# Kernel tuning notes

Measured on AMD Instinct MI355X. Metric: run time of the kernel, lower is better.

The kernel has to match this reference:

```python
import jax, jax.numpy as jnp
import numpy as np

B, T, D = 4, 4096, 512
H, L = 8, 6
HD = D // H
BS = 64          # block_size
MLP = 2048
VOCAB = 96000
MAX_SCALE = 10000.0
LN_EPS = 1e-6


def _sinusoidal_pe(length, dim, max_scale=MAX_SCALE):
    # flax common_layers sinusoidal init (concat sin|cos halves)
    pos = np.arange(length)[:, None].astype(np.float32)
    div = np.exp(np.arange(0, dim, 2).astype(np.float32) * -(np.log(max_scale) / dim))
    pe = np.zeros((length, dim), dtype=np.float32)
    pe[:, : dim // 2] = np.sin(pos * div)
    pe[:, dim // 2:] = np.cos(pos * div)
    return jnp.asarray(pe)

_PE = _sinusoidal_pe(T, D)


def layer_norm(x, scale, bias):
    m = jnp.mean(x, axis=-1, keepdims=True)
    v = jnp.mean(jnp.square(x - m), axis=-1, keepdims=True)
    return (x - m) * jax.lax.rsqrt(v + LN_EPS) * scale + bias


def local_block_attention(x, mask, wq, wk, wv, wo, stagger):
    # x: [B, T, D], mask: [B, T] bool (True = real token)
    b, t, d = x.shape
    if stagger:
        lp = BS // 2
        rp = BS - lp
        x = jnp.pad(x, ((0, 0), (lp, rp), (0, 0)))
        mask = jnp.pad(mask, ((0, 0), (lp, rp)))
    tp = x.shape[1]
    nb = tp // BS
    xb = x.reshape(b, nb, BS, d)          # [B, nb, BS, D]
    mb = mask.reshape(b, nb, BS)          # [B, nb, BS]
    scale = 1.0 / float(np.sqrt(HD))
    q = jnp.einsum('bnsd,dhf->bnshf', xb, wq) * scale
    k = jnp.einsum('bnsd,dhf->bnshf', xb, wk)
    v = jnp.einsum('bnsd,dhf->bnshf', xb, wv)
    scores = jnp.einsum('bnqhf,bnkhf->bnhqk', q, k)       # [B, nb, H, BS, BS]
    scores = jnp.where(mb[:, :, None, None, :], scores, jnp.asarray(-1e9, scores.dtype))
    probs = jax.nn.softmax(scores, axis=-1)
    o = jnp.einsum('bnhqk,bnkhf->bnqhf', probs, v)
    o = jnp.einsum('bnqhf,hfd->bnqd', o, wo).reshape(b, tp, d)
    if stagger:
        o = o[:, lp:lp + t]
    return o


def setup_inputs() -> dict:
    key = jax.random.key(0)
    ks = jax.random.split(key, 10)
    inputs = jax.random.randint(ks[0], (B, T), 0, VOCAB)
    embed = jax.random.normal(ks[1], (VOCAB, D), dtype=jnp.float32)
    s = 0.02
    wq = jax.random.normal(ks[2], (L, D, H, HD), dtype=jnp.float32) * s
    wk = jax.random.normal(ks[3], (L, D, H, HD), dtype=jnp.float32) * s
    wv = jax.random.normal(ks[4], (L, D, H, HD), dtype=jnp.float32) * s
    wo = jax.random.normal(ks[5], (L, H, HD, D), dtype=jnp.float32) * s
    w1 = jax.random.normal(ks[6], (L, D, MLP), dtype=jnp.float32) * s
    b1 = jnp.zeros((L, MLP), dtype=jnp.float32)
    w2 = jax.random.normal(ks[7], (L, MLP, D), dtype=jnp.float32) * s
    b2 = jnp.zeros((L, D), dtype=jnp.float32)
    ln1_s = jnp.ones((L, D), dtype=jnp.float32)
    ln1_b = jnp.zeros((L, D), dtype=jnp.float32)
    ln2_s = jnp.ones((L, D), dtype=jnp.float32)
    ln2_b = jnp.zeros((L, D), dtype=jnp.float32)
    lnf_s = jnp.ones((D,), dtype=jnp.float32)
    lnf_b = jnp.zeros((D,), dtype=jnp.float32)
    return {'inputs': inputs, 'embed': embed, 'wq': wq, 'wk': wk, 'wv': wv, 'wo': wo,
            'ln1_s': ln1_s, 'ln1_b': ln1_b, 'ln2_s': ln2_s, 'ln2_b': ln2_b,
            'w1': w1, 'b1': b1, 'w2': w2, 'b2': b2, 'lnf_s': lnf_s, 'lnf_b': lnf_b}


def reference(inputs, embed, wq, wk, wv, wo, ln1_s, ln1_b, ln2_s, ln2_b,
              w1, b1, w2, b2, lnf_s, lnf_b):
    mask = inputs > 0                      # src padding mask [B, T]
    x = embed[inputs.astype(jnp.int32)]    # [B, T, D]
    x = x + _PE[None, :, :]                # sinusoidal position embedding
    for lyr in range(L):
        stagger = (lyr % 2 == 1)           # stagger_local_blocks on odd layers
        h = layer_norm(x, ln1_s[lyr], ln1_b[lyr])
        h = local_block_attention(h, mask, wq[lyr], wk[lyr], wv[lyr], wo[lyr], stagger)
        x = x + h
        y = layer_norm(x, ln2_s[lyr], ln2_b[lyr])
        y = jnp.matmul(jax.nn.relu(jnp.matmul(y, w1[lyr]) + b1[lyr]), w2[lyr]) + b2[lyr]
        x = x + y
    return layer_norm(x, lnf_s, lnf_b)
```

## Files before the change

kernel.cpp:

```cpp
#include <hip/hip_runtime.h>

typedef unsigned short u16;
typedef unsigned int   u32;
typedef __attribute__((ext_vector_type(8))) short short8;
typedef __attribute__((ext_vector_type(4))) float f32x4;

#define TSEQ   4096
#define DMODEL 512
#define NHEAD  8
#define HDIM   64
#define NLAYER 6
#define MLPD   2048

#define GPTR(p) (const __attribute__((address_space(1))) void*)(p)
#define LPTR(p) (__attribute__((address_space(3))) void*)(p)

__device__ __forceinline__ u16 f2b(float f) {
  u32 u = __float_as_uint(f);
  u32 r = (u + 0x7fffu + ((u >> 16) & 1u)) >> 16;
  return (u16)r;
}
__device__ __forceinline__ float b2f(u16 h) { return __uint_as_float(((u32)h) << 16); }

__device__ __forceinline__ short8 ld8g(const u16* p, bool ok) {
  if (ok) return *(const short8*)p;
  short8 z = {0, 0, 0, 0, 0, 0, 0, 0};
  return z;
}

__global__ __launch_bounds__(256) void transpose_convert_all(
    const float* __restrict__ wq, const float* __restrict__ wk,
    const float* __restrict__ wv, const float* __restrict__ wo,
    const float* __restrict__ w1, const float* __restrict__ w2,
    u16* __restrict__ wqkv_bt, u16* __restrict__ wo_bt,
    u16* __restrict__ w1_bt, u16* __restrict__ w2_bt) {
  __shared__ float tile[64][65];
  int bx = blockIdx.x, l = blockIdx.y;
  const float* W; u16* out; int K, N, Ntot, ro, kb, nb2;
  if (bx < 256) {
    int which = bx >> 6, local = bx & 63;
    K = 512; N = 512; kb = local & 7; nb2 = local >> 3;
    if (which == 0)      { W = wq; out = wqkv_bt; Ntot = 1536; ro = 0; }
    else if (which == 1) { W = wk; out = wqkv_bt; Ntot = 1536; ro = 512; }
    else if (which == 2) { W = wv; out = wqkv_bt; Ntot = 1536; ro = 1024; }
    else                 { W = wo; out = wo_bt;   Ntot = 512;  ro = 0; }
  } else if (bx < 512) {
    int local = bx - 256;
    W = w1; out = w1_bt; K = 512; N = 2048; Ntot = 2048; ro = 0;
    kb = local & 7; nb2 = local >> 3;
  } else {
    int local = bx - 512;
    W = w2; out = w2_bt; K = 2048; N = 512; Ntot = 512; ro = 0;
    kb = local >> 3; nb2 = local & 7;
  }
  int k0 = kb * 64, n0 = nb2 * 64;
  const float* Wl = W + (size_t)l * K * N;
  u16* Ol = out + (size_t)l * Ntot * K;
  int tx = threadIdx.x & 15, ty = threadIdx.x >> 4;
#pragma unroll
  for (int p = 0; p < 4; ++p) {
    int k = k0 + p * 16 + ty;
    float4 v = *(const float4*)(Wl + (size_t)k * N + n0 + tx * 4);
    tile[p * 16 + ty][tx * 4 + 0] = v.x;
    tile[p * 16 + ty][tx * 4 + 1] = v.y;
    tile[p * 16 + ty][tx * 4 + 2] = v.z;
    tile[p * 16 + ty][tx * 4 + 3] = v.w;
  }
  __syncthreads();
#pragma unroll
  for (int p = 0; p < 4; ++p) {
    int n = n0 + p * 16 + ty;
    ushort4 s;
    s.x = f2b(tile[tx * 4 + 0][p * 16 + ty]);
    s.y = f2b(tile[tx * 4 + 1][p * 16 + ty]);
    s.z = f2b(tile[tx * 4 + 2][p * 16 + ty]);
    s.w = f2b(tile[tx * 4 + 3][p * 16 + ty]);
    *(ushort4*)(Ol + (size_t)(ro + n) * K + k0 + tx * 4) = s;
  }
}

__global__ void embed_pe_kernel(const int* __restrict__ idx,
                                const float* __restrict__ embed,
                                float* __restrict__ x) {
  int i = blockIdx.x;
  int t = i & (TSEQ - 1);
  int tok = idx[i];
  int c = threadIdx.x * 4;
  float4 e = *(const float4*)(embed + (size_t)tok * DMODEL + c);
  float vals[4] = {e.x, e.y, e.z, e.w};
  float o[4];
#pragma unroll
  for (int j = 0; j < 4; ++j) {
    int col = c + j;
    int jj = (col < 256) ? col : col - 256;
    float div = __expf((float)jj * -0.035977892078032f);
    float arg = (float)t * div;
    o[j] = vals[j] + ((col < 256) ? __sinf(arg) : __cosf(arg));
  }
  float4 r = {o[0], o[1], o[2], o[3]};
  *(float4*)(x + (size_t)i * DMODEL + c) = r;
}

template <bool OUT_BF16>
__global__ __launch_bounds__(256) void ln_kernel(
    const float* __restrict__ x, const float* __restrict__ gamma,
    const float* __restrict__ beta, void* __restrict__ out) {
  int wave = threadIdx.x >> 6, lane = threadIdx.x & 63;
  int row = (blockIdx.x << 2) + wave;
  const float* xr = x + (size_t)row * DMODEL + lane * 8;
  float4 a = *(const float4*)xr;
  float4 b = *(const float4*)(xr + 4);
  float v[8] = {a.x, a.y, a.z, a.w, b.x, b.y, b.z, b.w};
  float s = 0.f;
#pragma unroll
  for (int j = 0; j < 8; ++j) s += v[j];
#pragma unroll
  for (int off = 1; off < 64; off <<= 1) s += __shfl_xor(s, off, 64);
  float mean = s * (1.0f / 512.0f);
  float q = 0.f;
#pragma unroll
  for (int j = 0; j < 8; ++j) { float d = v[j] - mean; q += d * d; }
#pragma unroll
  for (int off = 1; off < 64; off <<= 1) q += __shfl_xor(q, off, 64);
  float rstd = rsqrtf(q * (1.0f / 512.0f) + 1e-6f);
  float4 g0 = *(const float4*)(gamma + lane * 8);
  float4 g1 = *(const float4*)(gamma + lane * 8 + 4);
  float4 p0 = *(const float4*)(beta + lane * 8);
  float4 p1 = *(const float4*)(beta + lane * 8 + 4);
  float g[8] = {g0.x, g0.y, g0.z, g0.w, g1.x, g1.y, g1.z, g1.w};
  float be[8] = {p0.x, p0.y, p0.z, p0.w, p1.x, p1.y, p1.z, p1.w};
  float r[8];
#pragma unroll
  for (int j = 0; j < 8; ++j) r[j] = (v[j] - mean) * rstd * g[j] + be[j];
  if (OUT_BF16) {
    uint4 pk;
    pk.x = (u32)f2b(r[0]) | ((u32)f2b(r[1]) << 16);
    pk.y = (u32)f2b(r[2]) | ((u32)f2b(r[3]) << 16);
    pk.z = (u32)f2b(r[4]) | ((u32)f2b(r[5]) << 16);
    pk.w = (u32)f2b(r[6]) | ((u32)f2b(r[7]) << 16);
    *(uint4*)((u16*)out + (size_t)row * DMODEL + lane * 8) = pk;
  } else {
    float4 r0 = {r[0], r[1], r[2], r[3]};
    float4 r1 = {r[4], r[5], r[6], r[7]};
    float* op = (float*)out + (size_t)row * DMODEL + lane * 8;
    *(float4*)op = r0;
    *(float4*)(op + 4) = r1;
  }
}

template <int FLAGS>
__global__ __launch_bounds__(256) void gemm_kernel(
    const u16* __restrict__ A, const u16* __restrict__ Bt,
    const float* __restrict__ bias, const float* __restrict__ resid,
    void* __restrict__ out, void* __restrict__ out2, int M, int N, int K) {
  __shared__ __align__(16) u16 a_lds[128][32];
  __shared__ __align__(16) u16 b_lds[128][32];
  int m0 = blockIdx.y * 128, n0 = blockIdx.x * 128;
  int t = threadIdx.x;
  int lr = t >> 2, lc = (t & 3) * 8;
  int wave = t >> 6, lane = t & 63;
  int wm = (wave >> 1) * 64, wn = (wave & 1) * 64;
  int fr = lane & 15, quad = lane >> 4;

  f32x4 acc[4][4];
  f32x4 zz = {0.f, 0.f, 0.f, 0.f};
#pragma unroll
  for (int i = 0; i < 4; ++i)
#pragma unroll
    for (int j = 0; j < 4; ++j) acc[i][j] = zz;

  const u16* Ag0 = A + (size_t)(m0 + lr) * K + lc;
  const u16* Ag1 = A + (size_t)(m0 + lr + 64) * K + lc;
  const u16* Bg0 = Bt + (size_t)(n0 + lr) * K + lc;
  const u16* Bg1 = Bt + (size_t)(n0 + lr + 64) * K + lc;
  u16* lA0 = &a_lds[lr][lc];
  u16* lA1 = &a_lds[lr + 64][lc];
  u16* lB0 = &b_lds[lr][lc];
  u16* lB1 = &b_lds[lr + 64][lc];

  for (int k0 = 0; k0 < K; k0 += 32) {
    __syncthreads();
    __builtin_amdgcn_global_load_lds(GPTR(Ag0 + k0), LPTR(lA0), 16, 0, 0);
    __builtin_amdgcn_global_load_lds(GPTR(Ag1 + k0), LPTR(lA1), 16, 0, 0);
    __builtin_amdgcn_global_load_lds(GPTR(Bg0 + k0), LPTR(lB0), 16, 0, 0);
    __builtin_amdgcn_global_load_lds(GPTR(Bg1 + k0), LPTR(lB1), 16, 0, 0);
    __syncthreads();
    short8 af[4], bf[4];
#pragma unroll
    for (int mi = 0; mi < 4; ++mi)
      af[mi] = *(const short8*)&a_lds[wm + mi * 16 + fr][quad * 8];
#pragma unroll
    for (int ni = 0; ni < 4; ++ni)
      bf[ni] = *(const short8*)&b_lds[wn + ni * 16 + fr][quad * 8];
#pragma unroll
    for (int mi = 0; mi < 4; ++mi)
#pragma unroll
      for (int ni = 0; ni < 4; ++ni)
        acc[mi][ni] = __builtin_amdgcn_mfma_f32_16x16x32_bf16(
            af[mi], bf[ni], acc[mi][ni], 0, 0, 0);
  }

  if (FLAGS & 16) {
#pragma unroll
    for (int mi = 0; mi < 4; ++mi)
#pragma unroll
      for (int ni = 0; ni < 4; ++ni) {
        int colg = n0 + wn + ni * 16 + fr;
        if (colg < 1024) {
#pragma unroll
          for (int r = 0; r < 4; ++r) {
            int rowg = m0 + wm + mi * 16 + quad * 4 + r;
            ((u16*)out)[(size_t)rowg * 1024 + colg] = f2b(acc[mi][ni][r]);
          }
        } else {
          int hh = (colg - 1024) >> 6, ff = colg & 63;
          int rowg0 = m0 + wm + mi * 16 + quad * 4;
          int bb = rowg0 >> 12, tok = rowg0 & 4095;
          ushort4 pk;
          pk.x = f2b(acc[mi][ni][0]);
          pk.y = f2b(acc[mi][ni][1]);
          pk.z = f2b(acc[mi][ni][2]);
          pk.w = f2b(acc[mi][ni][3]);
          *(ushort4*)((u16*)out2 +
                      ((size_t)(bb * 8 + hh) * 64 + ff) * 4096 + tok) = pk;
        }
      }
    return;
  }

#pragma unroll
  for (int mi = 0; mi < 4; ++mi)
#pragma unroll
    for (int ni = 0; ni < 4; ++ni) {
      int colg = n0 + wn + ni * 16 + fr;
      float bv = (FLAGS & 1) ? bias[colg] : 0.0f;
#pragma unroll
      for (int r = 0; r < 4; ++r) {
        int rowg = m0 + wm + mi * 16 + quad * 4 + r;
        float val = acc[mi][ni][r] + bv;
        if (FLAGS & 2) val = fmaxf(val, 0.0f);
        if (FLAGS & 4) val += resid[(size_t)rowg * N + colg];
        if (FLAGS & 8)
          ((u16*)out)[(size_t)rowg * N + colg] = f2b(val);
        else
          ((float*)out)[(size_t)rowg * N + colg] = val;
      }
    }
}

__global__ __launch_bounds__(128) void attn_mfma_kernel(
    const u16* __restrict__ qk, const u16* __restrict__ vt,
    const int* __restrict__ tokens, u16* __restrict__ o, int sh) {
  __shared__ __align__(16) u16 ps[2][64][72];
  __shared__ float kmask[64];
  int n = blockIdx.x, hg = blockIdx.y, b = blockIdx.z;
  int tid = threadIdx.x;
  int w = tid >> 6, lane = tid & 63;
  int head = hg * 2 + w;
  int fr = lane & 15, quad = lane >> 4;

  if (tid < 64) {
    int pp = n * 64 + tid - sh;
    kmask[tid] =
        (pp >= 0 && pp < TSEQ && tokens[(size_t)b * TSEQ + pp] > 0) ? 1.f : 0.f;
  }
  __syncthreads();

  const u16* qkb = qk + (size_t)b * TSEQ * 1024;

  f32x4 st[4][4];
  f32x4 zz = {0.f, 0.f, 0.f, 0.f};
#pragma unroll
  for (int i = 0; i < 4; ++i)
#pragma unroll
    for (int j = 0; j < 4; ++j) st[i][j] = zz;
#pragma unroll
  for (int kk = 0; kk < 2; ++kk) {
    short8 ka[4], qb[4];
#pragma unroll
    for (int mi = 0; mi < 4; ++mi) {
      int p = n * 64 + mi * 16 + fr - sh;
      ka[mi] = ld8g(qkb + (ptrdiff_t)p * 1024 + 512 + head * 64 + kk * 32 + quad * 8,
                    p >= 0 && p < TSEQ);
    }
#pragma unroll
    for (int ni = 0; ni < 4; ++ni) {
      int p = n * 64 + ni * 16 + fr - sh;
      qb[ni] = ld8g(qkb + (ptrdiff_t)p * 1024 + head * 64 + kk * 32 + quad * 8,
                    p >= 0 && p < TSEQ);
    }
#pragma unroll
    for (int mi = 0; mi < 4; ++mi)
#pragma unroll
      for (int ni = 0; ni < 4; ++ni)
        st[mi][ni] = __builtin_amdgcn_mfma_f32_16x16x32_bf16(
            ka[mi], qb[ni], st[mi][ni], 0, 0, 0);
  }

  float kmv[4][4];
#pragma unroll
  for (int mi = 0; mi < 4; ++mi)
#pragma unroll
    for (int r = 0; r < 4; ++r) kmv[mi][r] = kmask[mi * 16 + quad * 4 + r];
#pragma unroll
  for (int ni = 0; ni < 4; ++ni) {
    float mx = -3.0e38f;
#pragma unroll
    for (int mi = 0; mi < 4; ++mi)
#pragma unroll
      for (int r = 0; r < 4; ++r) {
        float s = (kmv[mi][r] > 0.f) ? st[mi][ni][r] * 0.125f : -1.0e9f;
        st[mi][ni][r] = s;
        mx = fmaxf(mx, s);
      }
    mx = fmaxf(mx, __shfl_xor(mx, 16, 64));
    mx = fmaxf(mx, __shfl_xor(mx, 32, 64));
    float sm = 0.f;
#pragma unroll
    for (int mi = 0; mi < 4; ++mi)
#pragma unroll
      for (int r = 0; r < 4; ++r) {
        float e = __expf(st[mi][ni][r] - mx);
        st[mi][ni][r] = e;
        sm += e;
      }
    sm += __shfl_xor(sm, 16, 64);
    sm += __shfl_xor(sm, 32, 64);
    float inv = 1.0f / sm;
#pragma unroll
    for (int mi = 0; mi < 4; ++mi)
#pragma unroll
      for (int r = 0; r < 4; ++r) st[mi][ni][r] *= inv;
  }

#pragma unroll
  for (int mi = 0; mi < 4; ++mi)
#pragma unroll
    for (int ni = 0; ni < 4; ++ni) {
      uint2 pk;
      pk.x = (u32)f2b(st[mi][ni][0]) | ((u32)f2b(st[mi][ni][1]) << 16);
      pk.y = (u32)f2b(st[mi][ni][2]) | ((u32)f2b(st[mi][ni][3]) << 16);
      *(uint2*)&ps[w][ni * 16 + fr][mi * 16 + quad * 4] = pk;
    }
  __syncthreads();

  f32x4 oc[4][4];
#pragma unroll
  for (int i = 0; i < 4; ++i)
#pragma unroll
    for (int j = 0; j < 4; ++j) oc[i][j] = zz;
  const u16* vtb = vt + (size_t)(b * 8 + head) * 64 * 4096;
#pragma unroll
  for (int kk = 0; kk < 2; ++kk) {
    short8 pa[4], vb[4];
#pragma unroll
    for (int mi = 0; mi < 4; ++mi)
      pa[mi] = *(const short8*)&ps[w][mi * 16 + fr][kk * 32 + quad * 8];
    int key0 = n * 64 - sh + kk * 32 + quad * 8;
    bool kok = (key0 >= 0) && (key0 < TSEQ);
#pragma unroll
    for (int ni = 0; ni < 4; ++ni)
      vb[ni] = ld8g(vtb + (size_t)(ni * 16 + fr) * 4096 + key0, kok);
#pragma unroll
    for (int mi = 0; mi < 4; ++mi)
#pragma unroll
      for (int ni = 0; ni < 4; ++ni)
        oc[mi][ni] = __builtin_amdgcn_mfma_f32_16x16x32_bf16(
            pa[mi], vb[ni], oc[mi][ni], 0, 0, 0);
  }

#pragma unroll
  for (int mi = 0; mi < 4; ++mi)
#pragma unroll
    for (int ni = 0; ni < 4; ++ni)
#pragma unroll
      for (int r = 0; r < 4; ++r) {
        int q = mi * 16 + quad * 4 + r;
        int p = n * 64 + q - sh;
        if (p >= 0 && p < TSEQ)
          o[((size_t)(b * TSEQ + p)) * DMODEL + head * 64 + ni * 16 + fr] =
              f2b(oc[mi][ni][r]);
      }
}

extern "C" void kernel_launch(void* const* d_in, const int* in_sizes, int n_in,
                              void* d_out, int out_size, void* d_ws, size_t ws_size,
                              hipStream_t stream) {
  (void)in_sizes; (void)n_in; (void)out_size; (void)ws_size;
  const int*   tokens = (const int*)d_in[0];
  const float* embed  = (const float*)d_in[1];
  const float* wq = (const float*)d_in[2];
  const float* wk = (const float*)d_in[3];
  const float* wv = (const float*)d_in[4];
  const float* wo = (const float*)d_in[5];
  const float* ln1_s = (const float*)d_in[6];
  const float* ln1_b = (const float*)d_in[7];
  const float* ln2_s = (const float*)d_in[8];
  const float* ln2_b = (const float*)d_in[9];
  const float* w1 = (const float*)d_in[10];
  const float* b1 = (const float*)d_in[11];
  const float* w2 = (const float*)d_in[12];
  const float* b2 = (const float*)d_in[13];
  const float* lnf_s = (const float*)d_in[14];
  const float* lnf_b = (const float*)d_in[15];

  char* ws = (char*)d_ws;
  const size_t MB = 1024ull * 1024ull;
  float* x     = (float*)(ws + 0);
  u16* h       = (u16*)(ws + 32 * MB);
  u16* qk      = (u16*)(ws + 48 * MB);
  u16* vt      = (u16*)(ws + 82 * MB);
  u16* obuf    = (u16*)(ws + 99 * MB);
  u16* hidden  = (u16*)(ws + 48 * MB);
  u16* wqkv_bt = (u16*)(ws + 116 * MB);
  u16* wo_bt   = (u16*)(ws + 126 * MB);
  u16* w1_bt   = (u16*)(ws + 130 * MB);
  u16* w2_bt   = (u16*)(ws + 143 * MB);

  transpose_convert_all<<<dim3(768, 6), 256, 0, stream>>>(
      wq, wk, wv, wo, w1, w2, wqkv_bt, wo_bt, w1_bt, w2_bt);

  embed_pe_kernel<<<16384, 128, 0, stream>>>(tokens, embed, x);

  for (int l = 0; l < NLAYER; ++l) {
    int sh = (l & 1) ? 32 : 0;
    int nb = (l & 1) ? 65 : 64;
    ln_kernel<true><<<4096, 256, 0, stream>>>(x, ln1_s + l * 512, ln1_b + l * 512, h);
    gemm_kernel<16><<<dim3(12, 128), 256, 0, stream>>>(
        h, wqkv_bt + (size_t)l * 1536 * 512, nullptr, nullptr, qk, vt,
        16384, 1536, 512);
    attn_mfma_kernel<<<dim3(nb, 4, 4), 128, 0, stream>>>(qk, vt, tokens, obuf, sh);
    gemm_kernel<4><<<dim3(4, 128), 256, 0, stream>>>(
        obuf, wo_bt + (size_t)l * 512 * 512, nullptr, x, x, nullptr,
        16384, 512, 512);
    ln_kernel<true><<<4096, 256, 0, stream>>>(x, ln2_s + l * 512, ln2_b + l * 512, h);
    gemm_kernel<1 | 2 | 8><<<dim3(16, 128), 256, 0, stream>>>(
        h, w1_bt + (size_t)l * 2048 * 512, b1 + l * 2048, nullptr, hidden, nullptr,
        16384, 2048, 512);
    gemm_kernel<1 | 4><<<dim3(4, 128), 256, 0, stream>>>(
        hidden, w2_bt + (size_t)l * 512 * 2048, b2 + l * 512, x, x, nullptr,
        16384, 512, 2048);
  }
  ln_kernel<false><<<4096, 256, 0, stream>>>(x, lnf_s, lnf_b, d_out);
}
```

Measured before the change: 1.628 ms.

## Triple-buffer GEMM LDS tiles to overlap global loads with MFMA

The GEMM main loop now uses three LDS buffers and issues the global-to-LDS loads for the next K tile before computing the current one. A single s_waitcnt vmcnt(4) plus barrier per iteration replaces the two __syncthreads. This is meant to hide global memory latency behind MFMA work, at the cost of tripling LDS use per block, which may lower occupancy. Correctness depends on the vmcnt counting matching the four outstanding loads and on the third buffer guarding against write-after-read hazards.

```diff
diff --git a/kernel.cpp b/kernel.cpp
--- a/kernel.cpp
+++ b/kernel.cpp
@@ -153,8 +153,8 @@
     const u16* __restrict__ A, const u16* __restrict__ Bt,
     const float* __restrict__ bias, const float* __restrict__ resid,
     void* __restrict__ out, void* __restrict__ out2, int M, int N, int K) {
-  __shared__ __align__(16) u16 a_lds[128][32];
-  __shared__ __align__(16) u16 b_lds[128][32];
+  __shared__ __align__(16) u16 a_lds[3][128][32];
+  __shared__ __align__(16) u16 b_lds[3][128][32];
   int m0 = blockIdx.y * 128, n0 = blockIdx.x * 128;
   int t = threadIdx.x;
   int lr = t >> 2, lc = (t & 3) * 8;
@@ -173,31 +173,40 @@
   const u16* Ag1 = A + (size_t)(m0 + lr + 64) * K + lc;
   const u16* Bg0 = Bt + (size_t)(n0 + lr) * K + lc;
   const u16* Bg1 = Bt + (size_t)(n0 + lr + 64) * K + lc;
-  u16* lA0 = &a_lds[lr][lc];
-  u16* lA1 = &a_lds[lr + 64][lc];
-  u16* lB0 = &b_lds[lr][lc];
-  u16* lB1 = &b_lds[lr + 64][lc];
-
-  for (int k0 = 0; k0 < K; k0 += 32) {
-    __syncthreads();
-    __builtin_amdgcn_global_load_lds(GPTR(Ag0 + k0), LPTR(lA0), 16, 0, 0);
-    __builtin_amdgcn_global_load_lds(GPTR(Ag1 + k0), LPTR(lA1), 16, 0, 0);
-    __builtin_amdgcn_global_load_lds(GPTR(Bg0 + k0), LPTR(lB0), 16, 0, 0);
-    __builtin_amdgcn_global_load_lds(GPTR(Bg1 + k0), LPTR(lB1), 16, 0, 0);
-    __syncthreads();
+
+  __builtin_amdgcn_global_load_lds(GPTR(Ag0), LPTR(&a_lds[0][lr][lc]), 16, 0, 0);
+  __builtin_amdgcn_global_load_lds(GPTR(Ag1), LPTR(&a_lds[0][lr + 64][lc]), 16, 0, 0);
+  __builtin_amdgcn_global_load_lds(GPTR(Bg0), LPTR(&b_lds[0][lr][lc]), 16, 0, 0);
+  __builtin_amdgcn_global_load_lds(GPTR(Bg1), LPTR(&b_lds[0][lr + 64][lc]), 16, 0, 0);
+
+  int T = K >> 5;
+  int buf = 0;
+  for (int tt = 0; tt < T; ++tt) {
+    int nb = buf + 1 == 3 ? 0 : buf + 1;
+    if (tt + 1 < T) {
+      int off = (tt + 1) << 5;
+      __builtin_amdgcn_global_load_lds(GPTR(Ag0 + off), LPTR(&a_lds[nb][lr][lc]), 16, 0, 0);
+      __builtin_amdgcn_global_load_lds(GPTR(Ag1 + off), LPTR(&a_lds[nb][lr + 64][lc]), 16, 0, 0);
+      __builtin_amdgcn_global_load_lds(GPTR(Bg0 + off), LPTR(&b_lds[nb][lr][lc]), 16, 0, 0);
+      __builtin_amdgcn_global_load_lds(GPTR(Bg1 + off), LPTR(&b_lds[nb][lr + 64][lc]), 16, 0, 0);
+      asm volatile("s_waitcnt vmcnt(4)\n\ts_barrier" ::: "memory");
+    } else {
+      asm volatile("s_waitcnt vmcnt(0)\n\ts_barrier" ::: "memory");
+    }
     short8 af[4], bf[4];
 #pragma unroll
     for (int mi = 0; mi < 4; ++mi)
-      af[mi] = *(const short8*)&a_lds[wm + mi * 16 + fr][quad * 8];
+      af[mi] = *(const short8*)&a_lds[buf][wm + mi * 16 + fr][quad * 8];
 #pragma unroll
     for (int ni = 0; ni < 4; ++ni)
-      bf[ni] = *(const short8*)&b_lds[wn + ni * 16 + fr][quad * 8];
+      bf[ni] = *(const short8*)&b_lds[buf][wn + ni * 16 + fr][quad * 8];
 #pragma unroll
     for (int mi = 0; mi < 4; ++mi)
 #pragma unroll
       for (int ni = 0; ni < 4; ++ni)
         acc[mi][ni] = __builtin_amdgcn_mfma_f32_16x16x32_bf16(
             af[mi], bf[ni], acc[mi][ni], 0, 0, 0);
+    buf = nb;
   }
 
   if (FLAGS & 16) {
```

Result: faster. 1.567 ms (-3.8%).
